# Kernel optimization log

Hardware: AMD Instinct MI355X
Metric: run time of the kernel (lower is better)

## Reference

```python
import jax, jax.numpy as jnp
import numpy as np

B, N, FIN, H, D = 8, 2048, 64, 4, 32
ALPHA = 0.2  # LeakyReLU negative slope


def setup_inputs() -> dict:
    key = jax.random.key(0)
    k1, k2, k3, k4 = jax.random.split(key, 4)
    h = jax.random.normal(k1, (B, N, FIN), dtype=jnp.float32)
    adj = jax.random.randint(k2, (B, N, N), 0, 2).astype(jnp.int32)
    # ensure self-loops so every softmax row has at least one unmasked entry
    idx = jnp.arange(N)
    adj = adj.at[:, idx, idx].set(1)
    W = jax.random.normal(k3, (FIN, H * D), dtype=jnp.float32) * 0.1
    a = jax.random.normal(k4, (H, 2 * D), dtype=jnp.float32) * 0.1
    return {"h": h, "adj": adj, "W": W, "a": a}


def reference(h, adj, W, a):
    # h: (B,N,Fin), adj: (B,N,N) int, W: (Fin,H*D), a: (H,2D)
    Bn, Nn, _ = h.shape
    Hh, twoD = a.shape
    Dd = twoD // 2
    Wh = (h @ W).reshape(Bn, Nn, Hh, Dd).transpose(0, 2, 1, 3)  # (B,H,N,D)
    # e_ij = leakyrelu(Wh_i . a1 + Wh_j . a2) -- avoids O(N^2 * 2D) concat
    src = jnp.einsum('bhnd,hd->bhn', Wh, a[:, :Dd])  # (B,H,N)
    dst = jnp.einsum('bhnd,hd->bhn', Wh, a[:, Dd:])  # (B,H,N)
    e = jax.nn.leaky_relu(src[:, :, :, None] + dst[:, :, None, :], negative_slope=ALPHA)  # (B,H,N,N)
    e = jnp.where(adj[:, None, :, :] == 0, -jnp.inf, e)
    attn = jax.nn.softmax(e, axis=-1)  # (B,H,N,N)
    out = jnp.einsum('bhij,bhjd->bhid', attn, Wh)  # (B,H,N,D)
    return out.transpose(0, 2, 1, 3).reshape(Bn, Nn, Hh * Dd)
```

## Files before the change

kernel.cpp:

```cpp
#include <hip/hip_runtime.h>
#include <hip/hip_bf16.h>

typedef short short8 __attribute__((ext_vector_type(8)));
typedef float floatx4 __attribute__((ext_vector_type(4)));

#define B_   8
#define N_   2048
#define FIN_ 64
#define H_   4
#define D_   32
#define HD_  128
#define ALPHA_ 0.2f
#define LOG2E_ 1.4426950408889634f


__device__ __forceinline__ float fexp2(float x) {
#if __has_builtin(__builtin_amdgcn_exp2f)
    return __builtin_amdgcn_exp2f(x);
#else
    float r; asm("v_exp_f32 %0, %1" : "=v"(r) : "v"(x)); return r;
#endif
}

__device__ __forceinline__ unsigned pk2bf(float x, float y) {
#if __has_builtin(__builtin_amdgcn_cvt_pk_bf16_f32)
    auto p = __builtin_amdgcn_cvt_pk_bf16_f32(x, y);
    return __builtin_bit_cast(unsigned, p);
#else
    unsigned ux = __builtin_bit_cast(unsigned, x);
    ux = (ux + 0x7fffu + ((ux >> 16) & 1u)) >> 16;
    unsigned uy = __builtin_bit_cast(unsigned, y);
    uy = (uy + 0x7fffu + ((uy >> 16) & 1u)) >> 16;
    return ux | (uy << 16);
#endif
}

__global__ __launch_bounds__(256) void pack_adj(
    const int* __restrict__ adj, unsigned* __restrict__ packed)
{
    size_t gw = (size_t)blockIdx.x * 256 + threadIdx.x;
    const int4* p = (const int4*)(adj + gw * 32);
    unsigned w = 0;
    #pragma unroll
    for (int t = 0; t < 8; ++t) {
        int4 v = p[t];
        w |= ((unsigned)v.x << (4 * t))     | ((unsigned)v.y << (4 * t + 1)) |
             ((unsigned)v.z << (4 * t + 2)) | ((unsigned)v.w << (4 * t + 3));
    }
    packed[gw] = w;
}

__global__ __launch_bounds__(256) void gat_prep2(
    const float* __restrict__ h, const float* __restrict__ W, const float* __restrict__ a,
    unsigned short* __restrict__ WhT, float* __restrict__ src, unsigned short* __restrict__ dstb)
{
    __shared__ float Ws[FIN_][HD_];
    __shared__ float hsT[FIN_][36];
    int bx = blockIdx.x;
    int b = bx >> 6;
    int n0 = (bx & 63) * 32;
    int tid = threadIdx.x;

    #pragma unroll
    for (int it = 0; it < 8; ++it) {
        int idx = it * 256 + tid;
        int k = idx >> 5, c4 = (idx & 31) << 2;
        *(float4*)&Ws[k][c4] = *(const float4*)&W[k * HD_ + c4];
    }
    #pragma unroll
    for (int it = 0; it < 8; ++it) {
        int idx = it * 256 + tid;
        int r = idx >> 6, k = idx & 63;
        hsT[k][r] = h[((size_t)b * N_ + n0 + r) * FIN_ + k];
    }
    __syncthreads();

    int c = tid & 127;
    int rq = tid >> 7;
    float acc[16];
    #pragma unroll
    for (int r = 0; r < 16; ++r) acc[r] = 0.f;
    for (int k = 0; k < FIN_; ++k) {
        float wv = Ws[k][c];
        float4 h0 = *(const float4*)&hsT[k][rq * 16];
        float4 h1 = *(const float4*)&hsT[k][rq * 16 + 4];
        float4 h2 = *(const float4*)&hsT[k][rq * 16 + 8];
        float4 h3 = *(const float4*)&hsT[k][rq * 16 + 12];
        acc[0]  += h0.x * wv; acc[1]  += h0.y * wv; acc[2]  += h0.z * wv; acc[3]  += h0.w * wv;
        acc[4]  += h1.x * wv; acc[5]  += h1.y * wv; acc[6]  += h1.z * wv; acc[7]  += h1.w * wv;
        acc[8]  += h2.x * wv; acc[9]  += h2.y * wv; acc[10] += h2.z * wv; acc[11] += h2.w * wv;
        acc[12] += h3.x * wv; acc[13] += h3.y * wv; acc[14] += h3.z * wv; acc[15] += h3.w * wv;
    }

    __attribute__((aligned(16))) unsigned pk[8];
    #pragma unroll
    for (int q = 0; q < 8; ++q) pk[q] = pk2bf(acc[2 * q], acc[2 * q + 1]);
    unsigned short* wrow = WhT + ((size_t)b * HD_ + c) * N_ + n0 + rq * 16;
    *(uint4*)wrow       = *(uint4*)&pk[0];
    *(uint4*)(wrow + 8) = *(uint4*)&pk[4];

    int hh = c >> 5, d = c & 31;
    float a1v = a[hh * 64 + d];
    float a2v = a[hh * 64 + 32 + d];
    #pragma unroll
    for (int r = 0; r < 16; ++r) {
        float s1 = acc[r] * a1v;
        float s2 = acc[r] * a2v;
        #pragma unroll
        for (int off = 16; off >= 1; off >>= 1) {
            s1 += __shfl_xor(s1, off, 32);
            s2 += __shfl_xor(s2, off, 32);
        }
        if (d == 0) {
            int n = n0 + rq * 16 + r;
            src[(b * H_ + hh) * N_ + n] = s1 * LOG2E_;
            unsigned u = __builtin_bit_cast(unsigned, s2 * LOG2E_);
            u = (u + 0x7fffu + ((u >> 16) & 1u)) >> 16;
            dstb[(b * H_ + hh) * N_ + n] = (unsigned short)u;
        }
    }
}

__global__ __launch_bounds__(256) void gat_main3(
    const unsigned* __restrict__ packed, const unsigned short* __restrict__ WhT,
    const float* __restrict__ src, const unsigned short* __restrict__ dstb,
    float* __restrict__ out)
{
    __shared__ unsigned short dsts[H_ * N_];
    __shared__ unsigned adjW[16][68];

    int bx = blockIdx.x;
    int b = bx >> 7;
    int i0 = (bx & 127) * 16;
    int tid = threadIdx.x;

    #pragma unroll
    for (int it = 0; it < 4; ++it) {
        int idx = it * 256 + tid;
        *(uint4*)&dsts[idx * 8] = *(const uint4*)&dstb[(size_t)b * H_ * N_ + idx * 8];
    }
    {
        int row = tid >> 4, c4 = (tid & 15) * 4;
        *(int4*)&adjW[row][c4] =
            *(const int4*)&packed[((size_t)b * N_ + i0 + row) * 64 + c4];
    }

    int h = tid >> 6, l = tid & 63, g = l >> 4, m = l & 15;
    int g8 = g << 3;
    float src_r = src[(b * H_ + h) * N_ + i0 + m];
    const unsigned short* WhR0 = WhT + ((size_t)(b * H_ + h) * 32 + m) * N_;
    const unsigned short* WhR1 = WhR0 + (size_t)16 * N_;
    const unsigned short* dstH = &dsts[h * N_];

    short8 ones;
    #pragma unroll
    for (int q = 0; q < 8; ++q) ones[q] = (short)0x3F80;

    floatx4 acc0 = {0.f, 0.f, 0.f, 0.f};
    floatx4 acc1 = {0.f, 0.f, 0.f, 0.f};
    floatx4 acc2 = {0.f, 0.f, 0.f, 0.f};
    __syncthreads();

    for (int jc = 0; jc < N_; jc += 64) {
        #pragma unroll
        for (int k2 = 0; k2 < 2; ++k2) {
            int j0 = jc + (k2 << 5) + g8;
            unsigned word = adjW[m][(jc >> 5) + k2];
            unsigned sh = word >> g8;
            uint4 dv = *(const uint4*)&dstH[j0];
            short8 bf0 = *(const short8*)&WhR0[j0];
            short8 bf1 = *(const short8*)&WhR1[j0];
            const unsigned* du = (const unsigned*)&dv;
            float wv[8];
            #pragma unroll
            for (int c2 = 0; c2 < 4; ++c2) {
                float dlo = __builtin_bit_cast(float, du[c2] << 16);
                float dhi = __builtin_bit_cast(float, du[c2] & 0xffff0000u);
                float e0 = src_r + dlo;
                float e1 = src_r + dhi;
                e0 = fmaxf(e0, ALPHA_ * e0);
                e1 = fmaxf(e1, ALPHA_ * e1);
                float x0 = fexp2(e0);
                float x1 = fexp2(e1);
                wv[2 * c2]     = (sh & (1u << (2 * c2))) ? x0 : 0.f;
                wv[2 * c2 + 1] = (sh & (2u << (2 * c2))) ? x1 : 0.f;
            }
            union { unsigned u[4]; short8 s; } U;
            #pragma unroll
            for (int q = 0; q < 4; ++q) U.u[q] = pk2bf(wv[2 * q], wv[2 * q + 1]);
            short8 af = U.s;
            acc0 = __builtin_amdgcn_mfma_f32_16x16x32_bf16(af, bf0, acc0, 0, 0, 0);
            acc1 = __builtin_amdgcn_mfma_f32_16x16x32_bf16(af, bf1, acc1, 0, 0, 0);
            acc2 = __builtin_amdgcn_mfma_f32_16x16x32_bf16(af, ones, acc2, 0, 0, 0);
        }
    }

    #pragma unroll
    for (int r = 0; r < 4; ++r) {
        float inv = __builtin_amdgcn_rcpf(acc2[r]);
        size_t o = ((size_t)b * N_ + i0 + g * 4 + r) * HD_ + h * 32 + m;
        out[o]      = acc0[r] * inv;
        out[o + 16] = acc1[r] * inv;
    }
}

extern "C" void kernel_launch(void* const* d_in, const int* in_sizes, int n_in,
                              void* d_out, int out_size, void* d_ws, size_t ws_size,
                              hipStream_t stream) {
    const float* h   = (const float*)d_in[0];
    const int*   adj = (const int*)d_in[1];
    const float* W   = (const float*)d_in[2];
    const float* a   = (const float*)d_in[3];
    float* out = (float*)d_out;

    unsigned*       packed = (unsigned*)d_ws;
    unsigned short* WhT    = (unsigned short*)((char*)d_ws + 4u * 1024 * 1024);
    float*          src    = (float*)((char*)d_ws + 8u * 1024 * 1024);
    unsigned short* dstb   = (unsigned short*)((char*)d_ws + 8u * 1024 * 1024 + 256u * 1024);

    pack_adj<<<(B_ * N_ * (N_ / 32)) / 256, 256, 0, stream>>>(adj, packed);
    gat_prep2<<<B_ * (N_ / 32), 256, 0, stream>>>(h, W, a, WhT, src, dstb);
    gat_main3<<<B_ * (N_ / 16), 256, 0, stream>>>(packed, WhT, src, dstb, out);
}
```

Baseline: 271.4 us.

## Split neighbor dimension across two blocks with partial sums and a finalize kernel

The attention kernel now splits the neighbor (j) range into two halves, so twice as many blocks run. Each block writes unnormalized partial outputs and softmax denominators to workspace, and a new finalize kernel sums the halves and divides. Two smaller changes go with it: the loop prefetches the next Wh fragment one iteration ahead, and the kernel declares 8-wave occupancy now that its LDS footprint is halved. The cost is an extra launch plus roughly 16 MB of partial results written and read back through global memory.

```diff
diff --git a/kernel.cpp b/kernel.cpp
--- a/kernel.cpp
+++ b/kernel.cpp
@@ -121,36 +121,41 @@
     }
 }
 
-__global__ __launch_bounds__(256) void gat_main3(
+__global__ __launch_bounds__(256, 8) void gat_main4(
     const unsigned* __restrict__ packed, const unsigned short* __restrict__ WhT,
     const float* __restrict__ src, const unsigned short* __restrict__ dstb,
-    float* __restrict__ out)
-{
-    __shared__ unsigned short dsts[H_ * N_];
-    __shared__ unsigned adjW[16][68];
+    float* __restrict__ pO, float* __restrict__ pW)
+{
+    __shared__ unsigned short dsts[H_ * 1024];
+    __shared__ unsigned adjW[16][36];
 
     int bx = blockIdx.x;
-    int b = bx >> 7;
-    int i0 = (bx & 127) * 16;
+    int b    = bx >> 8;
+    int rest = bx & 255;
+    int half = rest & 1;
+    int i0   = (rest >> 1) * 16;
+    int jb   = half << 10;
     int tid = threadIdx.x;
 
     #pragma unroll
-    for (int it = 0; it < 4; ++it) {
+    for (int it = 0; it < 2; ++it) {
         int idx = it * 256 + tid;
-        *(uint4*)&dsts[idx * 8] = *(const uint4*)&dstb[(size_t)b * H_ * N_ + idx * 8];
-    }
-    {
-        int row = tid >> 4, c4 = (tid & 15) * 4;
+        int hh = idx >> 7, off = (idx & 127) * 8;
+        *(uint4*)&dsts[hh * 1024 + off] =
+            *(const uint4*)&dstb[(size_t)(b * H_ + hh) * N_ + jb + off];
+    }
+    if (tid < 128) {
+        int row = tid >> 3, c4 = (tid & 7) * 4;
         *(int4*)&adjW[row][c4] =
-            *(const int4*)&packed[((size_t)b * N_ + i0 + row) * 64 + c4];
+            *(const int4*)&packed[((size_t)b * N_ + i0 + row) * 64 + (half << 5) + c4];
     }
 
     int h = tid >> 6, l = tid & 63, g = l >> 4, m = l & 15;
     int g8 = g << 3;
     float src_r = src[(b * H_ + h) * N_ + i0 + m];
-    const unsigned short* WhR0 = WhT + ((size_t)(b * H_ + h) * 32 + m) * N_;
+    const unsigned short* WhR0 = WhT + ((size_t)(b * H_ + h) * 32 + m) * N_ + jb;
     const unsigned short* WhR1 = WhR0 + (size_t)16 * N_;
-    const unsigned short* dstH = &dsts[h * N_];
+    const unsigned short* dstH = &dsts[h * 1024];
 
     short8 ones;
     #pragma unroll
@@ -161,47 +166,75 @@
     floatx4 acc2 = {0.f, 0.f, 0.f, 0.f};
     __syncthreads();
 
-    for (int jc = 0; jc < N_; jc += 64) {
-        #pragma unroll
-        for (int k2 = 0; k2 < 2; ++k2) {
-            int j0 = jc + (k2 << 5) + g8;
-            unsigned word = adjW[m][(jc >> 5) + k2];
-            unsigned sh = word >> g8;
-            uint4 dv = *(const uint4*)&dstH[j0];
-            short8 bf0 = *(const short8*)&WhR0[j0];
-            short8 bf1 = *(const short8*)&WhR1[j0];
-            const unsigned* du = (const unsigned*)&dv;
-            float wv[8];
-            #pragma unroll
-            for (int c2 = 0; c2 < 4; ++c2) {
-                float dlo = __builtin_bit_cast(float, du[c2] << 16);
-                float dhi = __builtin_bit_cast(float, du[c2] & 0xffff0000u);
-                float e0 = src_r + dlo;
-                float e1 = src_r + dhi;
-                e0 = fmaxf(e0, ALPHA_ * e0);
-                e1 = fmaxf(e1, ALPHA_ * e1);
-                float x0 = fexp2(e0);
-                float x1 = fexp2(e1);
-                wv[2 * c2]     = (sh & (1u << (2 * c2))) ? x0 : 0.f;
-                wv[2 * c2 + 1] = (sh & (2u << (2 * c2))) ? x1 : 0.f;
-            }
-            union { unsigned u[4]; short8 s; } U;
-            #pragma unroll
-            for (int q = 0; q < 4; ++q) U.u[q] = pk2bf(wv[2 * q], wv[2 * q + 1]);
-            short8 af = U.s;
-            acc0 = __builtin_amdgcn_mfma_f32_16x16x32_bf16(af, bf0, acc0, 0, 0, 0);
-            acc1 = __builtin_amdgcn_mfma_f32_16x16x32_bf16(af, bf1, acc1, 0, 0, 0);
-            acc2 = __builtin_amdgcn_mfma_f32_16x16x32_bf16(af, ones, acc2, 0, 0, 0);
+    short8 bf0_c = *(const short8*)&WhR0[g8];
+    short8 bf1_c = *(const short8*)&WhR1[g8];
+
+    for (int it = 0; it < 32; ++it) {
+        int j0 = (it << 5) + g8;
+        short8 bf0_n = *(const short8*)&WhR0[j0 + 32];
+        short8 bf1_n = *(const short8*)&WhR1[j0 + 32];
+
+        unsigned sh = adjW[m][it] >> g8;
+        uint4 dv = *(const uint4*)&dstH[j0];
+        const unsigned* du = (const unsigned*)&dv;
+        float wv[8];
+        #pragma unroll
+        for (int c2 = 0; c2 < 4; ++c2) {
+            float dlo = __builtin_bit_cast(float, du[c2] << 16);
+            float dhi = __builtin_bit_cast(float, du[c2] & 0xffff0000u);
+            float e0 = src_r + dlo;
+            float e1 = src_r + dhi;
+            e0 = fmaxf(e0, ALPHA_ * e0);
+            e1 = fmaxf(e1, ALPHA_ * e1);
+            float x0 = fexp2(e0);
+            float x1 = fexp2(e1);
+            wv[2 * c2]     = (sh & (1u << (2 * c2))) ? x0 : 0.f;
+            wv[2 * c2 + 1] = (sh & (2u << (2 * c2))) ? x1 : 0.f;
         }
-    }
-
+        union { unsigned u[4]; short8 s; } U;
+        #pragma unroll
+        for (int q = 0; q < 4; ++q) U.u[q] = pk2bf(wv[2 * q], wv[2 * q + 1]);
+        short8 af = U.s;
+        acc0 = __builtin_amdgcn_mfma_f32_16x16x32_bf16(af, bf0_c, acc0, 0, 0, 0);
+        acc1 = __builtin_amdgcn_mfma_f32_16x16x32_bf16(af, bf1_c, acc1, 0, 0, 0);
+        acc2 = __builtin_amdgcn_mfma_f32_16x16x32_bf16(af, ones,  acc2, 0, 0, 0);
+        bf0_c = bf0_n;
+        bf1_c = bf1_n;
+    }
+
+    if (m == 0) {
+        #pragma unroll
+        for (int r = 0; r < 4; ++r)
+            pW[(((size_t)half * B_ + b) * H_ + h) * N_ + i0 + g * 4 + r] = acc2[r];
+    }
     #pragma unroll
     for (int r = 0; r < 4; ++r) {
-        float inv = __builtin_amdgcn_rcpf(acc2[r]);
-        size_t o = ((size_t)b * N_ + i0 + g * 4 + r) * HD_ + h * 32 + m;
-        out[o]      = acc0[r] * inv;
-        out[o + 16] = acc1[r] * inv;
-    }
+        size_t o = ((size_t)(half * B_ + b) * N_ + i0 + g * 4 + r) * HD_ + h * 32 + m;
+        pO[o]      = acc0[r];
+        pO[o + 16] = acc1[r];
+    }
+}
+
+__global__ __launch_bounds__(256) void gat_fin(
+    const float* __restrict__ pO, const float* __restrict__ pW, float* __restrict__ out)
+{
+    int gid = blockIdx.x * 256 + threadIdx.x;
+    int c4 = (gid & 31) << 2;
+    int i  = (gid >> 5) & (N_ - 1);
+    int b  = gid >> 16;
+    int hh = c4 >> 5;
+    float w0 = pW[((size_t)b * H_ + hh) * N_ + i];
+    float w1 = pW[(((size_t)B_ + b) * H_ + hh) * N_ + i];
+    float inv = 1.f / (w0 + w1);
+    size_t o = ((size_t)b * N_ + i) * HD_ + c4;
+    float4 v0 = *(const float4*)&pO[o];
+    float4 v1 = *(const float4*)&pO[(size_t)B_ * N_ * HD_ + o];
+    float4 r;
+    r.x = (v0.x + v1.x) * inv;
+    r.y = (v0.y + v1.y) * inv;
+    r.z = (v0.z + v1.z) * inv;
+    r.w = (v0.w + v1.w) * inv;
+    *(float4*)&out[o] = r;
 }
 
 extern "C" void kernel_launch(void* const* d_in, const int* in_sizes, int n_in,
@@ -217,8 +250,11 @@
     unsigned short* WhT    = (unsigned short*)((char*)d_ws + 4u * 1024 * 1024);
     float*          src    = (float*)((char*)d_ws + 8u * 1024 * 1024);
     unsigned short* dstb   = (unsigned short*)((char*)d_ws + 8u * 1024 * 1024 + 256u * 1024);
+    float*          pO     = (float*)((char*)d_ws + 12u * 1024 * 1024);
+    float*          pW     = (float*)((char*)d_ws + 28u * 1024 * 1024);
 
     pack_adj<<<(B_ * N_ * (N_ / 32)) / 256, 256, 0, stream>>>(adj, packed);
     gat_prep2<<<B_ * (N_ / 32), 256, 0, stream>>>(h, W, a, WhT, src, dstb);
-    gat_main3<<<B_ * (N_ / 16), 256, 0, stream>>>(packed, WhT, src, dstb, out);
-}
+    gat_main4<<<B_ * (N_ / 16) * 2, 256, 0, stream>>>(packed, WhT, src, dstb, pO, pW);
+    gat_fin<<<(B_ * N_ * HD_ / 4) / 256, 256, 0, stream>>>(pO, pW, out);
+}
```

After: 276.1 us. Within noise of the previous version (+1.7%).

## Fuse adjacency bit-packing into main attention kernel with prefetched ballot masks

Applied to the files above, without the earlier changes.

Removes the separate pack_adj kernel. The main kernel now reads the int32 adjacency directly, builds bitmasks with wave ballots into shared memory in four column chunks, and prefetches the next chunk's adjacency values while computing the current one. This avoids a kernel launch and the write and re-read of the packed adjacency buffer, overlapping the unavoidable 134MB adjacency read with compute. It costs 32 extra registers per thread, adds a launch-bounds occupancy hint, and puts four block-wide barriers in the main loop.

```diff
diff --git a/kernel.cpp b/kernel.cpp
--- a/kernel.cpp
+++ b/kernel.cpp
@@ -35,21 +35,6 @@
 #endif
 }
 
-__global__ __launch_bounds__(256) void pack_adj(
-    const int* __restrict__ adj, unsigned* __restrict__ packed)
-{
-    size_t gw = (size_t)blockIdx.x * 256 + threadIdx.x;
-    const int4* p = (const int4*)(adj + gw * 32);
-    unsigned w = 0;
-    #pragma unroll
-    for (int t = 0; t < 8; ++t) {
-        int4 v = p[t];
-        w |= ((unsigned)v.x << (4 * t))     | ((unsigned)v.y << (4 * t + 1)) |
-             ((unsigned)v.z << (4 * t + 2)) | ((unsigned)v.w << (4 * t + 3));
-    }
-    packed[gw] = w;
-}
-
 __global__ __launch_bounds__(256) void gat_prep2(
     const float* __restrict__ h, const float* __restrict__ W, const float* __restrict__ a,
     unsigned short* __restrict__ WhT, float* __restrict__ src, unsigned short* __restrict__ dstb)
@@ -121,8 +106,8 @@
     }
 }
 
-__global__ __launch_bounds__(256) void gat_main3(
-    const unsigned* __restrict__ packed, const unsigned short* __restrict__ WhT,
+__global__ __launch_bounds__(256, 4) void gat_main6(
+    const int* __restrict__ adj, const unsigned short* __restrict__ WhT,
     const float* __restrict__ src, const unsigned short* __restrict__ dstb,
     float* __restrict__ out)
 {
@@ -133,19 +118,24 @@
     int b = bx >> 7;
     int i0 = (bx & 127) * 16;
     int tid = threadIdx.x;
+    int wv = tid >> 6, l = tid & 63;
 
     #pragma unroll
     for (int it = 0; it < 4; ++it) {
         int idx = it * 256 + tid;
         *(uint4*)&dsts[idx * 8] = *(const uint4*)&dstb[(size_t)b * H_ * N_ + idx * 8];
     }
-    {
-        int row = tid >> 4, c4 = (tid & 15) * 4;
-        *(int4*)&adjW[row][c4] =
-            *(const int4*)&packed[((size_t)b * N_ + i0 + row) * 64 + c4];
-    }
-
-    int h = tid >> 6, l = tid & 63, g = l >> 4, m = l & 15;
+
+    const int* adjBase = adj + ((size_t)(b * N_ + i0 + wv * 4)) * N_ + l;
+
+    int vals[32];
+    #pragma unroll
+    for (int rr = 0; rr < 4; ++rr)
+        #pragma unroll
+        for (int cc = 0; cc < 8; ++cc)
+            vals[rr * 8 + cc] = adjBase[rr * N_ + cc * 64];
+
+    int h = wv, g = l >> 4, m = l & 15;
     int g8 = g << 3;
     float src_r = src[(b * H_ + h) * N_ + i0 + m];
     const unsigned short* WhR0 = WhT + ((size_t)(b * H_ + h) * 32 + m) * N_;
@@ -159,39 +149,61 @@
     floatx4 acc0 = {0.f, 0.f, 0.f, 0.f};
     floatx4 acc1 = {0.f, 0.f, 0.f, 0.f};
     floatx4 acc2 = {0.f, 0.f, 0.f, 0.f};
-    __syncthreads();
-
-    for (int jc = 0; jc < N_; jc += 64) {
+
+    for (int q = 0; q < 4; ++q) {
         #pragma unroll
-        for (int k2 = 0; k2 < 2; ++k2) {
-            int j0 = jc + (k2 << 5) + g8;
-            unsigned word = adjW[m][(jc >> 5) + k2];
-            unsigned sh = word >> g8;
-            uint4 dv = *(const uint4*)&dstH[j0];
-            short8 bf0 = *(const short8*)&WhR0[j0];
-            short8 bf1 = *(const short8*)&WhR1[j0];
-            const unsigned* du = (const unsigned*)&dv;
-            float wv[8];
+        for (int rr = 0; rr < 4; ++rr)
             #pragma unroll
-            for (int c2 = 0; c2 < 4; ++c2) {
-                float dlo = __builtin_bit_cast(float, du[c2] << 16);
-                float dhi = __builtin_bit_cast(float, du[c2] & 0xffff0000u);
-                float e0 = src_r + dlo;
-                float e1 = src_r + dhi;
-                e0 = fmaxf(e0, ALPHA_ * e0);
-                e1 = fmaxf(e1, ALPHA_ * e1);
-                float x0 = fexp2(e0);
-                float x1 = fexp2(e1);
-                wv[2 * c2]     = (sh & (1u << (2 * c2))) ? x0 : 0.f;
-                wv[2 * c2 + 1] = (sh & (2u << (2 * c2))) ? x1 : 0.f;
+            for (int cc = 0; cc < 8; ++cc) {
+                unsigned long long mk = __ballot(vals[rr * 8 + cc] != 0);
+                if (l == 0) {
+                    int c = q * 8 + cc;
+                    adjW[wv * 4 + rr][2 * c]     = (unsigned)mk;
+                    adjW[wv * 4 + rr][2 * c + 1] = (unsigned)(mk >> 32);
+                }
             }
-            union { unsigned u[4]; short8 s; } U;
+        __syncthreads();
+
+        if (q < 3) {
             #pragma unroll
-            for (int q = 0; q < 4; ++q) U.u[q] = pk2bf(wv[2 * q], wv[2 * q + 1]);
-            short8 af = U.s;
-            acc0 = __builtin_amdgcn_mfma_f32_16x16x32_bf16(af, bf0, acc0, 0, 0, 0);
-            acc1 = __builtin_amdgcn_mfma_f32_16x16x32_bf16(af, bf1, acc1, 0, 0, 0);
-            acc2 = __builtin_amdgcn_mfma_f32_16x16x32_bf16(af, ones, acc2, 0, 0, 0);
+            for (int rr = 0; rr < 4; ++rr)
+                #pragma unroll
+                for (int cc = 0; cc < 8; ++cc)
+                    vals[rr * 8 + cc] = adjBase[rr * N_ + (q + 1) * 512 + cc * 64];
+        }
+
+        for (int jj = 0; jj < 8; ++jj) {
+            #pragma unroll
+            for (int k2 = 0; k2 < 2; ++k2) {
+                int it = q * 16 + jj * 2 + k2;
+                int j0 = (it << 5) + g8;
+                unsigned sh = adjW[m][it] >> g8;
+                uint4 dv = *(const uint4*)&dstH[j0];
+                short8 bf0 = *(const short8*)&WhR0[j0];
+                short8 bf1 = *(const short8*)&WhR1[j0];
+                const unsigned* du = (const unsigned*)&dv;
+                float wvv[8];
+                #pragma unroll
+                for (int c2 = 0; c2 < 4; ++c2) {
+                    float dlo = __builtin_bit_cast(float, du[c2] << 16);
+                    float dhi = __builtin_bit_cast(float, du[c2] & 0xffff0000u);
+                    float e0 = src_r + dlo;
+                    float e1 = src_r + dhi;
+                    e0 = fmaxf(e0, ALPHA_ * e0);
+                    e1 = fmaxf(e1, ALPHA_ * e1);
+                    float x0 = fexp2(e0);
+                    float x1 = fexp2(e1);
+                    wvv[2 * c2]     = (sh & (1u << (2 * c2))) ? x0 : 0.f;
+                    wvv[2 * c2 + 1] = (sh & (2u << (2 * c2))) ? x1 : 0.f;
+                }
+                union { unsigned u[4]; short8 s; } U;
+                #pragma unroll
+                for (int p = 0; p < 4; ++p) U.u[p] = pk2bf(wvv[2 * p], wvv[2 * p + 1]);
+                short8 af = U.s;
+                acc0 = __builtin_amdgcn_mfma_f32_16x16x32_bf16(af, bf0, acc0, 0, 0, 0);
+                acc1 = __builtin_amdgcn_mfma_f32_16x16x32_bf16(af, bf1, acc1, 0, 0, 0);
+                acc2 = __builtin_amdgcn_mfma_f32_16x16x32_bf16(af, ones, acc2, 0, 0, 0);
+            }
         }
     }
 
@@ -213,12 +225,10 @@
     const float* a   = (const float*)d_in[3];
     float* out = (float*)d_out;
 
-    unsigned*       packed = (unsigned*)d_ws;
-    unsigned short* WhT    = (unsigned short*)((char*)d_ws + 4u * 1024 * 1024);
-    float*          src    = (float*)((char*)d_ws + 8u * 1024 * 1024);
-    unsigned short* dstb   = (unsigned short*)((char*)d_ws + 8u * 1024 * 1024 + 256u * 1024);
-
-    pack_adj<<<(B_ * N_ * (N_ / 32)) / 256, 256, 0, stream>>>(adj, packed);
+    unsigned short* WhT  = (unsigned short*)d_ws;
+    float*          src  = (float*)((char*)d_ws + 4u * 1024 * 1024);
+    unsigned short* dstb = (unsigned short*)((char*)d_ws + 4u * 1024 * 1024 + 256u * 1024);
+
     gat_prep2<<<B_ * (N_ / 32), 256, 0, stream>>>(h, W, a, WhT, src, dstb);
-    gat_main3<<<B_ * (N_ / 16), 256, 0, stream>>>(packed, WhT, src, dstb, out);
-}
+    gat_main6<<<B_ * (N_ / 16), 256, 0, stream>>>(adj, WhT, src, dstb, out);
+}
```

After: 257.6 us. 5.1% less time.
